# Kernel tuning notes

Measured on AMD Instinct MI355X. Metric: run time of the kernel, lower is better.

The kernel has to match this reference:

```python
import jax, jax.numpy as jnp
import numpy as np
from jax import lax

S, B, F, H = 2048, 512, 1, 128  # seq_len, minibatch, feature_count, mlp hidden


def setup_inputs() -> dict:
    key = jax.random.key(0)
    ks = jax.random.split(key, 7)
    x = jax.random.normal(ks[0], (S, B, F), dtype=jnp.float32)
    # derivative network: 2 -> H -> H -> 2 tanh MLP (ignores t, as in repo)
    W1 = jax.random.normal(ks[1], (2, H), dtype=jnp.float32) / np.sqrt(2.0)
    b1 = jnp.zeros((H,), dtype=jnp.float32)
    W2 = jax.random.normal(ks[2], (H, H), dtype=jnp.float32) / np.sqrt(H)
    b2 = jnp.zeros((H,), dtype=jnp.float32)
    W3 = jax.random.normal(ks[3], (H, 2), dtype=jnp.float32) / np.sqrt(H)
    b3 = jnp.zeros((2,), dtype=jnp.float32)
    return {"x": x, "W1": W1, "b1": b1, "W2": W2, "b2": b2, "W3": W3, "b3": b3}


def reference(x, W1, b1, W2, b2, W3, b3):
    # x: (S, B, 1). Per step n: v = [x_n, state] in R^2 per sequence,
    # one forward-Euler step with dt = (n) - (n-1) = 1.0:
    #   y1 = v + dt * f(v)
    # output_n = y1[..., 1]; state <- output_n. Strict sequential recurrence.
    def mlp(v):  # v: (B, 2)
        h = jnp.tanh(v @ W1 + b1)
        h = jnp.tanh(h @ W2 + b2)
        return h @ W3 + b3  # (B, 2)

    dt = jnp.float32(1.0)

    def step(state, x_n):  # state: (B,1), x_n: (B,1)
        v = jnp.concatenate([x_n, state], axis=1)  # (B, 2)
        y1 = v + dt * mlp(v)
        out = y1[:, 1:2]  # channel 1 of the 2-dim ODE state
        return out, out

    init = jnp.zeros((x.shape[1], 1), dtype=x.dtype)
    _, ys = lax.scan(step, init, x)  # (S, B, 1)
    return ys
```

## Files before the change

### kernel.cpp

```cpp
#include <hip/hip_runtime.h>

#define SEQ 2048
#define BATCH 512
#define HDIM 128

typedef float f32x2 __attribute__((ext_vector_type(2)));

__device__ __forceinline__ float fast_tanh(float x) {
    float e = __expf(2.0f * x);
    return fmaf(-2.0f, __builtin_amdgcn_rcpf(e + 1.0f), 1.0f);
}

template<int CTRL>
__device__ __forceinline__ float dpp_add(float x) {
    return x + __int_as_float(__builtin_amdgcn_update_dpp(
        0, __float_as_int(x), CTRL, 0xf, 0xf, false));
}

__global__ __launch_bounds__(256, 2)
void odenet_scan_kernel(const float* __restrict__ x,
                        const float* __restrict__ W1,
                        const float* __restrict__ b1,
                        const float* __restrict__ W2,
                        const float* __restrict__ b2,
                        const float* __restrict__ W3,
                        const float* __restrict__ b3,
                        float* __restrict__ out)
{
    const int t  = threadIdx.x;
    const int l  = t & 63;
    const int w  = t >> 6;
    const int pr = l >> 2;
    const int kq = l & 3;
    const int c0 = 32 * w + 2 * pr;
    const int b  = blockIdx.x;

    __shared__ float xbuf[SEQ];
    __shared__ float h1buf[4][4 * 36];
    __shared__ float ybuf[2][4];

    {
        float v[8];
        #pragma unroll
        for (int i = 0; i < 8; ++i)
            v[i] = x[(i * 256 + t) * BATCH + b];
        #pragma unroll
        for (int i = 0; i < 8; ++i)
            xbuf[i * 256 + t] = v[i];
    }

    f32x2 wA[16], wB[16];
    #pragma unroll
    for (int i = 0; i < 16; ++i) {
        const int k0 = 32 * kq + 2 * i;
        wA[i] = f32x2{W2[k0 * HDIM + c0],     W2[(k0 + 1) * HDIM + c0]};
        wB[i] = f32x2{W2[k0 * HDIM + c0 + 1], W2[(k0 + 1) * HDIM + c0 + 1]};
    }

    const float2 w1x = *reinterpret_cast<const float2*>(&W1[2 * l]);
    const float2 w1s = *reinterpret_cast<const float2*>(&W1[HDIM + 2 * l]);
    const float2 b1v = *reinterpret_cast<const float2*>(&b1[2 * l]);
    const float2 b2v = *reinterpret_cast<const float2*>(&b2[c0]);
    const float w3s0 = W3[(c0 + 0) * 2 + 1] * 0.25f;
    const float w3s1 = W3[(c0 + 1) * 2 + 1] * 0.25f;
    const float b31  = b3[1];

    const int hoff = 36 * (l >> 4) + ((2 * l) & 31);
    const float4* h4 = reinterpret_cast<const float4*>(&h1buf[w][36 * kq]);

    __syncthreads();

    float s = 0.0f;
    float s_hold = 0.0f;
    float xn = xbuf[0];

    for (int n = 0; n < SEQ; ++n) {
        const int par = n & 1;

        float ha = fast_tanh(fmaf(w1x.x, xn, fmaf(w1s.x, s, b1v.x)));
        float hb = fast_tanh(fmaf(w1x.y, xn, fmaf(w1s.y, s, b1v.y)));
        *reinterpret_cast<float2*>(&h1buf[w][hoff]) = make_float2(ha, hb);
        __builtin_amdgcn_wave_barrier();

        float xnext = xbuf[(n + 1) & (SEQ - 1)];

        f32x2 accA = {0.0f, 0.0f}, accB = {0.0f, 0.0f};
        #pragma unroll
        for (int i = 0; i < 8; ++i) {
            float4 hv = h4[i];
            f32x2 hp0 = {hv.x, hv.y};
            f32x2 hp1 = {hv.z, hv.w};
            accA = __builtin_elementwise_fma(wA[2 * i],     hp0, accA);
            accB = __builtin_elementwise_fma(wB[2 * i],     hp0, accB);
            accA = __builtin_elementwise_fma(wA[2 * i + 1], hp1, accA);
            accB = __builtin_elementwise_fma(wB[2 * i + 1], hp1, accB);
        }
        __builtin_amdgcn_wave_barrier();

        float p0 = accA.x + accA.y;
        float p1 = accB.x + accB.y;
        p0 = dpp_add<0xB1>(p0); p0 = dpp_add<0x4E>(p0);
        p1 = dpp_add<0xB1>(p1); p1 = dpp_add<0x4E>(p1);

        float z = fast_tanh(p0 + b2v.x) * w3s0;
        z = fmaf(fast_tanh(p1 + b2v.y), w3s1, z);

        z = dpp_add<0x111>(z);
        z = dpp_add<0x112>(z);
        z = dpp_add<0x114>(z);
        z = dpp_add<0x118>(z);
        z = dpp_add<0x142>(z);
        z = dpp_add<0x143>(z);

        if (l == 63) ybuf[par][w] = z;
        __syncthreads();

        const float4 yv = *reinterpret_cast<const float4*>(&ybuf[par][0]);
        s = s + ((yv.x + yv.y) + (yv.z + yv.w)) + b31;

        if (w == 0) {
            if (l == (n & 63)) s_hold = s;
            if ((n & 63) == 63) out[(n - 63 + l) * BATCH + b] = s_hold;
        }
        xn = xnext;
    }
}

extern "C" void kernel_launch(void* const* d_in, const int* in_sizes, int n_in,
                              void* d_out, int out_size, void* d_ws, size_t ws_size,
                              hipStream_t stream) {
    const float* x  = (const float*)d_in[0];
    const float* W1 = (const float*)d_in[1];
    const float* b1 = (const float*)d_in[2];
    const float* W2 = (const float*)d_in[3];
    const float* b2 = (const float*)d_in[4];
    const float* W3 = (const float*)d_in[5];
    const float* b3 = (const float*)d_in[6];
    float* out = (float*)d_out;

    dim3 grid(BATCH);
    dim3 block(256);
    odenet_scan_kernel<<<grid, block, 0, stream>>>(x, W1, b1, W2, b2, W3, b3, out);
}
```

Measured before the change: 1.063 ms.

## Process two batch sequences per block to amortize barriers and weight registers

Each 256-thread block now advances two independent sequences in lockstep instead of one, halving the grid to 256 blocks. The W2 weights held in registers are reused for both sequences, and the per-step block barrier and DPP reductions are shared across two recurrences, which adds instruction-level parallelism inside the latency-bound serial loop. In exchange the block handles twice the work per step, occupancy drops (launch bounds lowered to 1), and with 256 blocks some compute units may sit idle.

```diff
diff --git a/kernel.cpp b/kernel.cpp
--- a/kernel.cpp
+++ b/kernel.cpp
@@ -17,7 +17,7 @@
         0, __float_as_int(x), CTRL, 0xf, 0xf, false));
 }
 
-__global__ __launch_bounds__(256, 2)
+__global__ __launch_bounds__(256, 1)
 void odenet_scan_kernel(const float* __restrict__ x,
                         const float* __restrict__ W1,
                         const float* __restrict__ b1,
@@ -33,17 +33,17 @@
     const int pr = l >> 2;
     const int kq = l & 3;
     const int c0 = 32 * w + 2 * pr;
-    const int b  = blockIdx.x;
+    const int b0 = 2 * blockIdx.x;
 
-    __shared__ float xbuf[SEQ];
-    __shared__ float h1buf[4][4 * 36];
-    __shared__ float ybuf[2][4];
+    __shared__ float2 xbuf[SEQ];
+    __shared__ float  h1buf[4][2][4 * 36];
+    __shared__ float2 ybuf[2][4];
 
     {
-        float v[8];
+        float2 v[8];
         #pragma unroll
         for (int i = 0; i < 8; ++i)
-            v[i] = x[(i * 256 + t) * BATCH + b];
+            v[i] = *reinterpret_cast<const float2*>(&x[(i * 256 + t) * BATCH + b0]);
         #pragma unroll
         for (int i = 0; i < 8; ++i)
             xbuf[i * 256 + t] = v[i];
@@ -66,61 +66,80 @@
     const float b31  = b3[1];
 
     const int hoff = 36 * (l >> 4) + ((2 * l) & 31);
-    const float4* h4 = reinterpret_cast<const float4*>(&h1buf[w][36 * kq]);
+    const float4* hA4 = reinterpret_cast<const float4*>(&h1buf[w][0][36 * kq]);
+    const float4* hB4 = reinterpret_cast<const float4*>(&h1buf[w][1][36 * kq]);
 
     __syncthreads();
 
-    float s = 0.0f;
+    float sA = 0.0f, sB = 0.0f;
     float s_hold = 0.0f;
-    float xn = xbuf[0];
+    float2 xn = xbuf[0];
 
     for (int n = 0; n < SEQ; ++n) {
         const int par = n & 1;
 
-        float ha = fast_tanh(fmaf(w1x.x, xn, fmaf(w1s.x, s, b1v.x)));
-        float hb = fast_tanh(fmaf(w1x.y, xn, fmaf(w1s.y, s, b1v.y)));
-        *reinterpret_cast<float2*>(&h1buf[w][hoff]) = make_float2(ha, hb);
+        float haA = fast_tanh(fmaf(w1x.x, xn.x, fmaf(w1s.x, sA, b1v.x)));
+        float haB = fast_tanh(fmaf(w1x.x, xn.y, fmaf(w1s.x, sB, b1v.x)));
+        float hbA = fast_tanh(fmaf(w1x.y, xn.x, fmaf(w1s.y, sA, b1v.y)));
+        float hbB = fast_tanh(fmaf(w1x.y, xn.y, fmaf(w1s.y, sB, b1v.y)));
+        *reinterpret_cast<float2*>(&h1buf[w][0][hoff]) = make_float2(haA, hbA);
+        *reinterpret_cast<float2*>(&h1buf[w][1][hoff]) = make_float2(haB, hbB);
         __builtin_amdgcn_wave_barrier();
 
-        float xnext = xbuf[(n + 1) & (SEQ - 1)];
+        float2 xnext = xbuf[(n + 1) & (SEQ - 1)];
 
-        f32x2 accA = {0.0f, 0.0f}, accB = {0.0f, 0.0f};
+        f32x2 aA0 = {0.0f, 0.0f}, aA1 = {0.0f, 0.0f};
+        f32x2 aB0 = {0.0f, 0.0f}, aB1 = {0.0f, 0.0f};
         #pragma unroll
         for (int i = 0; i < 8; ++i) {
-            float4 hv = h4[i];
-            f32x2 hp0 = {hv.x, hv.y};
-            f32x2 hp1 = {hv.z, hv.w};
-            accA = __builtin_elementwise_fma(wA[2 * i],     hp0, accA);
-            accB = __builtin_elementwise_fma(wB[2 * i],     hp0, accB);
-            accA = __builtin_elementwise_fma(wA[2 * i + 1], hp1, accA);
-            accB = __builtin_elementwise_fma(wB[2 * i + 1], hp1, accB);
+            float4 hva = hA4[i];
+            float4 hvb = hB4[i];
+            f32x2 a0 = {hva.x, hva.y}, a1 = {hva.z, hva.w};
+            f32x2 bq0 = {hvb.x, hvb.y}, bq1 = {hvb.z, hvb.w};
+            aA0 = __builtin_elementwise_fma(wA[2 * i],     a0,  aA0);
+            aB0 = __builtin_elementwise_fma(wA[2 * i],     bq0, aB0);
+            aA1 = __builtin_elementwise_fma(wB[2 * i],     a0,  aA1);
+            aB1 = __builtin_elementwise_fma(wB[2 * i],     bq0, aB1);
+            aA0 = __builtin_elementwise_fma(wA[2 * i + 1], a1,  aA0);
+            aB0 = __builtin_elementwise_fma(wA[2 * i + 1], bq1, aB0);
+            aA1 = __builtin_elementwise_fma(wB[2 * i + 1], a1,  aA1);
+            aB1 = __builtin_elementwise_fma(wB[2 * i + 1], bq1, aB1);
         }
         __builtin_amdgcn_wave_barrier();
 
-        float p0 = accA.x + accA.y;
-        float p1 = accB.x + accB.y;
-        p0 = dpp_add<0xB1>(p0); p0 = dpp_add<0x4E>(p0);
-        p1 = dpp_add<0xB1>(p1); p1 = dpp_add<0x4E>(p1);
+        float pA0 = aA0.x + aA0.y, pA1 = aA1.x + aA1.y;
+        float pB0 = aB0.x + aB0.y, pB1 = aB1.x + aB1.y;
+        pA0 = dpp_add<0xB1>(pA0); pB0 = dpp_add<0xB1>(pB0);
+        pA1 = dpp_add<0xB1>(pA1); pB1 = dpp_add<0xB1>(pB1);
+        pA0 = dpp_add<0x4E>(pA0); pB0 = dpp_add<0x4E>(pB0);
+        pA1 = dpp_add<0x4E>(pA1); pB1 = dpp_add<0x4E>(pB1);
 
-        float z = fast_tanh(p0 + b2v.x) * w3s0;
-        z = fmaf(fast_tanh(p1 + b2v.y), w3s1, z);
+        float zA = fast_tanh(pA0 + b2v.x) * w3s0;
+        float zB = fast_tanh(pB0 + b2v.x) * w3s0;
+        zA = fmaf(fast_tanh(pA1 + b2v.y), w3s1, zA);
+        zB = fmaf(fast_tanh(pB1 + b2v.y), w3s1, zB);
 
-        z = dpp_add<0x111>(z);
-        z = dpp_add<0x112>(z);
-        z = dpp_add<0x114>(z);
-        z = dpp_add<0x118>(z);
-        z = dpp_add<0x142>(z);
-        z = dpp_add<0x143>(z);
+        zA = dpp_add<0x111>(zA); zB = dpp_add<0x111>(zB);
+        zA = dpp_add<0x112>(zA); zB = dpp_add<0x112>(zB);
+        zA = dpp_add<0x114>(zA); zB = dpp_add<0x114>(zB);
+        zA = dpp_add<0x118>(zA); zB = dpp_add<0x118>(zB);
+        zA = dpp_add<0x142>(zA); zB = dpp_add<0x142>(zB);
+        zA = dpp_add<0x143>(zA); zB = dpp_add<0x143>(zB);
 
-        if (l == 63) ybuf[par][w] = z;
+        if (l == 63) ybuf[par][w] = make_float2(zA, zB);
         __syncthreads();
 
-        const float4 yv = *reinterpret_cast<const float4*>(&ybuf[par][0]);
-        s = s + ((yv.x + yv.y) + (yv.z + yv.w)) + b31;
+        const float4 y01 = *reinterpret_cast<const float4*>(&ybuf[par][0]);
+        const float4 y23 = *reinterpret_cast<const float4*>(&ybuf[par][2]);
+        sA = sA + ((y01.x + y01.z) + (y23.x + y23.z)) + b31;
+        sB = sB + ((y01.y + y01.w) + (y23.y + y23.w)) + b31;
 
         if (w == 0) {
-            if (l == (n & 63)) s_hold = s;
-            if ((n & 63) == 63) out[(n - 63 + l) * BATCH + b] = s_hold;
+            if (l == (n & 63)) s_hold = sA;
+            if ((n & 63) == 63) out[(n - 63 + l) * BATCH + b0] = s_hold;
+        } else if (w == 1) {
+            if (l == (n & 63)) s_hold = sB;
+            if ((n & 63) == 63) out[(n - 63 + l) * BATCH + b0 + 1] = s_hold;
         }
         xn = xnext;
     }
@@ -138,7 +157,7 @@
     const float* b3 = (const float*)d_in[6];
     float* out = (float*)d_out;
 
-    dim3 grid(BATCH);
+    dim3 grid(BATCH / 2);
     dim3 block(256);
     odenet_scan_kernel<<<grid, block, 0, stream>>>(x, W1, b1, W2, b2, W3, b3, out);
 }
```

New measurement: 1.434 ms. 1.35x slower.

## Run each sequence on a single wavefront and drop block-wide barriers

Applied to the files above, without the earlier changes.

The kernel now uses one 64-lane wavefront per batch element instead of four. Each lane computes two full output columns of the hidden layer, so the cross-wave __syncthreads and LDS exchange of partial sums are replaced by an in-wave DPP reduction plus a readlane. To hold the whole 128x128 W2 slice, 192 values stay in registers and a quarter is staged in LDS and re-read every step. This removes per-step block synchronisation but makes each wave do four times the FMA work per step, with heavy register pressure and extra LDS traffic.

```diff
diff --git a/kernel.cpp b/kernel.cpp
--- a/kernel.cpp
+++ b/kernel.cpp
@@ -17,7 +17,7 @@
         0, __float_as_int(x), CTRL, 0xf, 0xf, false));
 }
 
-__global__ __launch_bounds__(256, 2)
+__global__ __launch_bounds__(64, 1)
 void odenet_scan_kernel(const float* __restrict__ x,
                         const float* __restrict__ W1,
                         const float* __restrict__ b1,
@@ -27,83 +27,83 @@
                         const float* __restrict__ b3,
                         float* __restrict__ out)
 {
-    const int t  = threadIdx.x;
-    const int l  = t & 63;
-    const int w  = t >> 6;
-    const int pr = l >> 2;
-    const int kq = l & 3;
-    const int c0 = 32 * w + 2 * pr;
-    const int b  = blockIdx.x;
+    const int l = threadIdx.x;
+    const int b = blockIdx.x;
+    const int cA = 2 * l;
+    const int cB = 2 * l + 1;
 
-    __shared__ float xbuf[SEQ];
-    __shared__ float h1buf[4][4 * 36];
-    __shared__ float ybuf[2][4];
+    __shared__ float  xbuf[SEQ];
+    __shared__ float4 wlds4[16][64];
+    __shared__ float  h1s[HDIM];
 
-    {
-        float v[8];
-        #pragma unroll
-        for (int i = 0; i < 8; ++i)
-            v[i] = x[(i * 256 + t) * BATCH + b];
-        #pragma unroll
-        for (int i = 0; i < 8; ++i)
-            xbuf[i * 256 + t] = v[i];
+    for (int i = 0; i < 32; ++i)
+        xbuf[i * 64 + l] = x[(i * 64 + l) * BATCH + b];
+    #pragma unroll
+    for (int g = 0; g < 16; ++g) {
+        float4 wv;
+        wv.x = W2[(4 * g + 0) * HDIM + cB];
+        wv.y = W2[(4 * g + 1) * HDIM + cB];
+        wv.z = W2[(4 * g + 2) * HDIM + cB];
+        wv.w = W2[(4 * g + 3) * HDIM + cB];
+        wlds4[g][l] = wv;
     }
-
-    f32x2 wA[16], wB[16];
+    f32x2 wA[64];
     #pragma unroll
-    for (int i = 0; i < 16; ++i) {
-        const int k0 = 32 * kq + 2 * i;
-        wA[i] = f32x2{W2[k0 * HDIM + c0],     W2[(k0 + 1) * HDIM + c0]};
-        wB[i] = f32x2{W2[k0 * HDIM + c0 + 1], W2[(k0 + 1) * HDIM + c0 + 1]};
-    }
+    for (int i = 0; i < 64; ++i)
+        wA[i] = f32x2{W2[(2 * i) * HDIM + cA], W2[(2 * i + 1) * HDIM + cA]};
+    f32x2 wB[32];
+    #pragma unroll
+    for (int i = 0; i < 32; ++i)
+        wB[i] = f32x2{W2[(64 + 2 * i) * HDIM + cB], W2[(64 + 2 * i + 1) * HDIM + cB]};
 
     const float2 w1x = *reinterpret_cast<const float2*>(&W1[2 * l]);
     const float2 w1s = *reinterpret_cast<const float2*>(&W1[HDIM + 2 * l]);
     const float2 b1v = *reinterpret_cast<const float2*>(&b1[2 * l]);
-    const float2 b2v = *reinterpret_cast<const float2*>(&b2[c0]);
-    const float w3s0 = W3[(c0 + 0) * 2 + 1] * 0.25f;
-    const float w3s1 = W3[(c0 + 1) * 2 + 1] * 0.25f;
+    const float2 b2v = *reinterpret_cast<const float2*>(&b2[2 * l]);
+    const float w3v0 = W3[2 * cA + 1];
+    const float w3v1 = W3[2 * cB + 1];
     const float b31  = b3[1];
-
-    const int hoff = 36 * (l >> 4) + ((2 * l) & 31);
-    const float4* h4 = reinterpret_cast<const float4*>(&h1buf[w][36 * kq]);
 
     __syncthreads();
 
     float s = 0.0f;
     float s_hold = 0.0f;
     float xn = xbuf[0];
+    const float4* h4 = reinterpret_cast<const float4*>(h1s);
 
     for (int n = 0; n < SEQ; ++n) {
-        const int par = n & 1;
-
         float ha = fast_tanh(fmaf(w1x.x, xn, fmaf(w1s.x, s, b1v.x)));
         float hb = fast_tanh(fmaf(w1x.y, xn, fmaf(w1s.y, s, b1v.y)));
-        *reinterpret_cast<float2*>(&h1buf[w][hoff]) = make_float2(ha, hb);
+        *reinterpret_cast<float2*>(&h1s[2 * l]) = make_float2(ha, hb);
         __builtin_amdgcn_wave_barrier();
 
         float xnext = xbuf[(n + 1) & (SEQ - 1)];
 
         f32x2 accA = {0.0f, 0.0f}, accB = {0.0f, 0.0f};
         #pragma unroll
-        for (int i = 0; i < 8; ++i) {
-            float4 hv = h4[i];
+        for (int g = 0; g < 32; ++g) {
+            float4 hv = h4[g];
             f32x2 hp0 = {hv.x, hv.y};
             f32x2 hp1 = {hv.z, hv.w};
-            accA = __builtin_elementwise_fma(wA[2 * i],     hp0, accA);
-            accB = __builtin_elementwise_fma(wB[2 * i],     hp0, accB);
-            accA = __builtin_elementwise_fma(wA[2 * i + 1], hp1, accA);
-            accB = __builtin_elementwise_fma(wB[2 * i + 1], hp1, accB);
+            accA = __builtin_elementwise_fma(wA[2 * g],     hp0, accA);
+            accA = __builtin_elementwise_fma(wA[2 * g + 1], hp1, accA);
+            if (g < 16) {
+                float4 wv = wlds4[g][l];
+                f32x2 w0 = {wv.x, wv.y};
+                f32x2 w1 = {wv.z, wv.w};
+                accB = __builtin_elementwise_fma(w0, hp0, accB);
+                accB = __builtin_elementwise_fma(w1, hp1, accB);
+            } else {
+                accB = __builtin_elementwise_fma(wB[2 * (g - 16)],     hp0, accB);
+                accB = __builtin_elementwise_fma(wB[2 * (g - 16) + 1], hp1, accB);
+            }
         }
         __builtin_amdgcn_wave_barrier();
 
-        float p0 = accA.x + accA.y;
-        float p1 = accB.x + accB.y;
-        p0 = dpp_add<0xB1>(p0); p0 = dpp_add<0x4E>(p0);
-        p1 = dpp_add<0xB1>(p1); p1 = dpp_add<0x4E>(p1);
-
-        float z = fast_tanh(p0 + b2v.x) * w3s0;
-        z = fmaf(fast_tanh(p1 + b2v.y), w3s1, z);
+        float pA = accA.x + accA.y;
+        float pB = accB.x + accB.y;
+        float z = fast_tanh(pA + b2v.x) * w3v0;
+        z = fmaf(fast_tanh(pB + b2v.y), w3v1, z);
 
         z = dpp_add<0x111>(z);
         z = dpp_add<0x112>(z);
@@ -111,17 +111,13 @@
         z = dpp_add<0x118>(z);
         z = dpp_add<0x142>(z);
         z = dpp_add<0x143>(z);
+        float y = __int_as_float(__builtin_amdgcn_readlane(__float_as_int(z), 63));
 
-        if (l == 63) ybuf[par][w] = z;
-        __syncthreads();
+        s = s + y + b31;
 
-        const float4 yv = *reinterpret_cast<const float4*>(&ybuf[par][0]);
-        s = s + ((yv.x + yv.y) + (yv.z + yv.w)) + b31;
+        if (l == (n & 63)) s_hold = s;
+        if ((n & 63) == 63) out[(n - 63 + l) * BATCH + b] = s_hold;
 
-        if (w == 0) {
-            if (l == (n & 63)) s_hold = s;
-            if ((n & 63) == 63) out[(n - 63 + l) * BATCH + b] = s_hold;
-        }
         xn = xnext;
     }
 }
@@ -139,6 +135,6 @@
     float* out = (float*)d_out;
 
     dim3 grid(BATCH);
-    dim3 block(256);
+    dim3 block(64);
     odenet_scan_kernel<<<grid, block, 0, stream>>>(x, W1, b1, W2, b2, W3, b3, out);
 }
```

Result: slower. 2.049 ms (+92.7%).

## Pack two batch sequences per 512-thread block and precompute input-layer term

Applied to the files above, without the earlier changes.

Each block now runs two independent sequences, one per group of four waves, so grid halves and block size doubles. The x loads become float2 and the x-dependent part of the first layer is computed one step ahead, off the recurrence critical path. DPP bound_ctrl is set and the two DPP chains are interleaved. The block-wide barrier now synchronizes eight waves per step, which may add barrier latency in exchange for fewer blocks and hidden per-step load and FMA latency.

```diff
diff --git a/kernel.cpp b/kernel.cpp
--- a/kernel.cpp
+++ b/kernel.cpp
@@ -14,10 +14,10 @@
 template<int CTRL>
 __device__ __forceinline__ float dpp_add(float x) {
     return x + __int_as_float(__builtin_amdgcn_update_dpp(
-        0, __float_as_int(x), CTRL, 0xf, 0xf, false));
+        0, __float_as_int(x), CTRL, 0xf, 0xf, true));
 }
 
-__global__ __launch_bounds__(256, 2)
+__global__ __launch_bounds__(512, 1)
 void odenet_scan_kernel(const float* __restrict__ x,
                         const float* __restrict__ W1,
                         const float* __restrict__ b1,
@@ -29,24 +29,26 @@
 {
     const int t  = threadIdx.x;
     const int l  = t & 63;
-    const int w  = t >> 6;
+    const int wv = t >> 6;
+    const int ch = wv >> 2;
+    const int w  = wv & 3;
     const int pr = l >> 2;
     const int kq = l & 3;
     const int c0 = 32 * w + 2 * pr;
-    const int b  = blockIdx.x;
+    const int b0 = 2 * blockIdx.x;
 
-    __shared__ float xbuf[SEQ];
-    __shared__ float h1buf[4][4 * 36];
-    __shared__ float ybuf[2][4];
+    __shared__ float2 xbuf[SEQ];
+    __shared__ float  h1buf[8][4 * 36];
+    __shared__ float  ybuf[2][8];
 
     {
-        float v[8];
+        float2 v[4];
         #pragma unroll
-        for (int i = 0; i < 8; ++i)
-            v[i] = x[(i * 256 + t) * BATCH + b];
+        for (int i = 0; i < 4; ++i)
+            v[i] = *reinterpret_cast<const float2*>(&x[(i * 512 + t) * BATCH + b0]);
         #pragma unroll
-        for (int i = 0; i < 8; ++i)
-            xbuf[i * 256 + t] = v[i];
+        for (int i = 0; i < 4; ++i)
+            xbuf[i * 512 + t] = v[i];
     }
 
     f32x2 wA[16], wB[16];
@@ -66,23 +68,27 @@
     const float b31  = b3[1];
 
     const int hoff = 36 * (l >> 4) + ((2 * l) & 31);
-    const float4* h4 = reinterpret_cast<const float4*>(&h1buf[w][36 * kq]);
+    const float4* h4 = reinterpret_cast<const float4*>(&h1buf[wv][36 * kq]);
 
     __syncthreads();
 
     float s = 0.0f;
     float s_hold = 0.0f;
-    float xn = xbuf[0];
+    float2 x0p = xbuf[0];
+    float xc = ch ? x0p.y : x0p.x;
+    float2 pre1 = make_float2(fmaf(w1x.x, xc, b1v.x), fmaf(w1x.y, xc, b1v.y));
 
     for (int n = 0; n < SEQ; ++n) {
         const int par = n & 1;
 
-        float ha = fast_tanh(fmaf(w1x.x, xn, fmaf(w1s.x, s, b1v.x)));
-        float hb = fast_tanh(fmaf(w1x.y, xn, fmaf(w1s.y, s, b1v.y)));
-        *reinterpret_cast<float2*>(&h1buf[w][hoff]) = make_float2(ha, hb);
+        float ha = fast_tanh(fmaf(w1s.x, s, pre1.x));
+        float hb = fast_tanh(fmaf(w1s.y, s, pre1.y));
+        *reinterpret_cast<float2*>(&h1buf[wv][hoff]) = make_float2(ha, hb);
         __builtin_amdgcn_wave_barrier();
 
-        float xnext = xbuf[(n + 1) & (SEQ - 1)];
+        float2 xnp = xbuf[(n + 1) & (SEQ - 1)];
+        float xn1 = ch ? xnp.y : xnp.x;
+        pre1 = make_float2(fmaf(w1x.x, xn1, b1v.x), fmaf(w1x.y, xn1, b1v.y));
 
         f32x2 accA = {0.0f, 0.0f}, accB = {0.0f, 0.0f};
         #pragma unroll
@@ -99,8 +105,8 @@
 
         float p0 = accA.x + accA.y;
         float p1 = accB.x + accB.y;
-        p0 = dpp_add<0xB1>(p0); p0 = dpp_add<0x4E>(p0);
-        p1 = dpp_add<0xB1>(p1); p1 = dpp_add<0x4E>(p1);
+        p0 = dpp_add<0xB1>(p0); p1 = dpp_add<0xB1>(p1);
+        p0 = dpp_add<0x4E>(p0); p1 = dpp_add<0x4E>(p1);
 
         float z = fast_tanh(p0 + b2v.x) * w3s0;
         z = fmaf(fast_tanh(p1 + b2v.y), w3s1, z);
@@ -112,17 +118,16 @@
         z = dpp_add<0x142>(z);
         z = dpp_add<0x143>(z);
 
-        if (l == 63) ybuf[par][w] = z;
+        if (l == 63) ybuf[par][wv] = z;
         __syncthreads();
 
-        const float4 yv = *reinterpret_cast<const float4*>(&ybuf[par][0]);
+        const float4 yv = *reinterpret_cast<const float4*>(&ybuf[par][4 * ch]);
         s = s + ((yv.x + yv.y) + (yv.z + yv.w)) + b31;
 
         if (w == 0) {
             if (l == (n & 63)) s_hold = s;
-            if ((n & 63) == 63) out[(n - 63 + l) * BATCH + b] = s_hold;
+            if ((n & 63) == 63) out[(n - 63 + l) * BATCH + b0 + ch] = s_hold;
         }
-        xn = xnext;
     }
 }
 
@@ -138,7 +143,7 @@
     const float* b3 = (const float*)d_in[6];
     float* out = (float*)d_out;
 
-    dim3 grid(BATCH);
-    dim3 block(256);
+    dim3 grid(BATCH / 2);
+    dim3 block(512);
     odenet_scan_kernel<<<grid, block, 0, stream>>>(x, W1, b1, W2, b2, W3, b3, out);
 }
```

New measurement: 1.057 ms. No clear change (-0.6%).
